# Kernel tuning notes

Measured on AMD Instinct MI355X. Metric: run time of the kernel, lower is better.

Reference implementation:

```python
import jax, jax.numpy as jnp
import numpy as np
import math

HEADS = 4
KV = 960
CH = (64, 128, 256, 512)
B, H, W = 8, 32, 32
EPS_IN = 1e-5  # nn.InstanceNorm2d default eps


def conv2d(x, w, groups=1, pad=0):
    # x: [N,C,H,W], w: [O, C//groups, kh, kw]
    return jax.lax.conv_general_dilated(
        x, w, (1, 1), [(pad, pad), (pad, pad)],
        feature_group_count=groups,
        dimension_numbers=('NCHW', 'OIHW', 'NCHW'))


def l2norm(x):
    # torch F.normalize(dim=-1): x / max(||x||_2, 1e-12)
    return x / jnp.maximum(jnp.linalg.norm(x, axis=-1, keepdims=True), 1e-12)


def setup_inputs() -> dict:
    key = jax.random.key(0)
    ks = iter(jax.random.split(key, 40))
    s = 0.02
    d = {}
    for i, c in enumerate(CH, 1):
        d[f'emb{i}'] = jax.random.normal(next(ks), (B, c, H, W), jnp.float32)
    d['emb_all'] = jax.random.normal(next(ks), (B, KV, H, W), jnp.float32)
    for i, c in enumerate(CH, 1):
        d[f'Wm{i}'] = jax.random.normal(next(ks), (c * HEADS, c, 1, 1), jnp.float32) * s
        # grouped 3x3: groups = c*HEADS//2 -> 2 in-channels per group
        d[f'Wq{i}'] = jax.random.normal(next(ks), (c * HEADS, 2, 3, 3), jnp.float32) * s
        d[f'Wp{i}'] = jax.random.normal(next(ks), (c, c, 1, 1), jnp.float32) * s
    d['Wmk'] = jax.random.normal(next(ks), (KV * HEADS, KV, 1, 1), jnp.float32) * s
    d['Wmv'] = jax.random.normal(next(ks), (KV * HEADS, KV, 1, 1), jnp.float32) * s
    # depthwise 3x3: groups = KV*HEADS
    d['Wk'] = jax.random.normal(next(ks), (KV * HEADS, 1, 3, 3), jnp.float32) * s
    d['Wv'] = jax.random.normal(next(ks), (KV * HEADS, 1, 3, 3), jnp.float32) * s
    return d


def _forward(emb1, emb2, emb3, emb4, emb_all,
             Wm1, Wq1, Wp1, Wm2, Wq2, Wp2, Wm3, Wq3, Wp3, Wm4, Wq4, Wp4,
             Wmk, Wmv, Wk, Wv):
    b, _, h, w = emb1.shape
    hw = h * w
    # shared K/V: 1x1 multi-head expand then depthwise 3x3
    k = conv2d(conv2d(emb_all, Wmk), Wk, groups=KV * HEADS, pad=1)
    v = conv2d(conv2d(emb_all, Wmv), Wv, groups=KV * HEADS, pad=1)
    k = l2norm(k.reshape(b, HEADS, KV, hw))   # [b,H,KV,hw]
    v = v.reshape(b, HEADS, KV, hw)
    scale = 1.0 / math.sqrt(KV)
    outs = []
    for emb, Wm, Wq, Wp in ((emb1, Wm1, Wq1, Wp1), (emb2, Wm2, Wq2, Wp2),
                            (emb3, Wm3, Wq3, Wp3), (emb4, Wm4, Wq4, Wp4)):
        c = emb.shape[1]
        q = conv2d(conv2d(emb, Wm), Wq, groups=c * HEADS // 2, pad=1)
        q = l2norm(q.reshape(b, HEADS, c, hw))            # [b,H,c,hw]
        attn = jnp.einsum('bhcn,bhdn->bhcd', q, k) * scale  # [b,H,c,KV]
        # InstanceNorm2d over (c, KV) per (b, head), no affine, biased var
        mu = attn.mean(axis=(2, 3), keepdims=True)
        var = attn.var(axis=(2, 3), keepdims=True)
        probs = jax.nn.softmax((attn - mu) / jnp.sqrt(var + EPS_IN), axis=-1)
        # dropout rate 0 (inference) -> identity
        out = jnp.einsum('bhcd,bhdn->bhcn', probs, v).mean(axis=1)  # head-mean -> [b,c,hw]
        outs.append(conv2d(out.reshape(b, c, h, w), Wp))
    return tuple(outs)


def reference(emb1, emb2, emb3, emb4, emb_all,
              Wm1, Wq1, Wp1, Wm2, Wq2, Wp2, Wm3, Wq3, Wp3, Wm4, Wq4, Wp4,
              Wmk, Wmv, Wk, Wv):
    return _forward(emb1, emb2, emb3, emb4, emb_all,
                    Wm1, Wq1, Wp1, Wm2, Wq2, Wp2, Wm3, Wq3, Wp3, Wm4, Wq4, Wp4,
                    Wmk, Wmv, Wk, Wv)
```

## Files before the change

kernel.cpp:

```cpp
#include <hip/hip_runtime.h>
#include <hip/hip_bf16.h>
#include <math.h>

typedef __hip_bfloat16 bf16;
typedef __attribute__((ext_vector_type(8))) short short8;
typedef __attribute__((ext_vector_type(8))) unsigned short u16x8;
typedef __attribute__((ext_vector_type(4))) float f32x4;
typedef long long ll;

#define B_ 8
#define HEADS_ 4
#define KV_ 960
#define HW_ 1024
#define CKV_ 3840

__device__ __forceinline__ float wredsum(float v) {
#pragma unroll
  for (int o = 32; o > 0; o >>= 1) v += __shfl_xor(v, o);
  return v;
}
__device__ __forceinline__ float wredmax(float v) {
#pragma unroll
  for (int o = 32; o > 0; o >>= 1) v = fmaxf(v, __shfl_xor(v, o));
  return v;
}

__device__ __forceinline__ float bfu2f(unsigned short u) {
  union { unsigned int i; float f; } c;
  c.i = ((unsigned int)u) << 16;
  return c.f;
}
__device__ __forceinline__ unsigned short f2bfu(float f) {
  bf16 h = __float2bfloat16(f);
  return *(unsigned short*)&h;
}

__device__ __forceinline__ void gl_lds16(const void* g, void* l) {
  __builtin_amdgcn_global_load_lds(
      (const __attribute__((address_space(1))) unsigned*)g,
      (__attribute__((address_space(3))) unsigned*)l, 16, 0, 0);
}

__global__ void __launch_bounds__(256) castw(const float* __restrict__ in,
                                             bf16* __restrict__ out, int n) {
  int i = (blockIdx.x * 256 + threadIdx.x) * 4;
  if (i < n) {
    float4 v = *(const float4*)(in + i);
    out[i] = __float2bfloat16(v.x);
    out[i + 1] = __float2bfloat16(v.y);
    out[i + 2] = __float2bfloat16(v.z);
    out[i + 3] = __float2bfloat16(v.w);
  }
}

template <typename InT>
__global__ void __launch_bounds__(256) tcast(const InT* __restrict__ in,
                                             bf16* __restrict__ out, int R,
                                             ll inZ, ll outZ) {
  __shared__ float t[32][33];
  const int x = threadIdx.x & 31, y0 = threadIdx.x >> 5;
  const int c0 = blockIdx.x << 5, r0 = blockIdx.y << 5;
  const InT* ip = in + (ll)blockIdx.z * inZ + (ll)r0 * 1024 + c0;
  bf16* op = out + (ll)blockIdx.z * outZ + (ll)c0 * R + r0;
#pragma unroll
  for (int i = 0; i < 4; i++) {
    int r = y0 + i * 8;
    float v;
    if constexpr (__is_same(InT, float)) v = ip[(ll)r * 1024 + x];
    else v = __bfloat162float(ip[(ll)r * 1024 + x]);
    t[r][x] = v;
  }
  __syncthreads();
#pragma unroll
  for (int i = 0; i < 4; i++) {
    int cc = y0 + i * 8;
    op[(ll)cc * R + x] = __float2bfloat16(t[x][cc]);
  }
}

template <int OUTMODE, bool STATS>
__global__ void __launch_bounds__(256) gemm_mfma(
    const bf16* __restrict__ A, const bf16* __restrict__ Bt, void* __restrict__ Y,
    int M, int N, int K, int nh,
    ll aZ, ll aH, ll bZ, ll bH, ll yZ, int ldy, float scale,
    float* __restrict__ part) {
  __shared__ bf16 As[2][128 * 32];
  __shared__ bf16 Bs[2][128 * 32];
  __shared__ float rs1[4], rs2[4];
  const int tid = threadIdx.x;
  const int lane = tid & 63;
  const int wave = tid >> 6;
  const int wr = wave >> 1, wc = wave & 1;

  const int gy = gridDim.y, gz = gridDim.z;
  int orig = (blockIdx.z * gy + blockIdx.y) * 8 + blockIdx.x;
  int cpx = (gy * gz);
  int flat = (orig & 7) * cpx + (orig >> 3);
  const int lx = flat & 7;
  int rest = flat >> 3;
  const int ly = rest % gy;
  const int lz = rest / gy;

  const int z = lz;
  const int m0 = ly << 7, n0 = lx << 7;

  f32x4 acc[4][4];
#pragma unroll
  for (int i = 0; i < 4; i++)
#pragma unroll
    for (int j = 0; j < 4; j++) acc[i][j] = (f32x4){0.f, 0.f, 0.f, 0.f};

  const int frow = lane & 15;
  const int kq = lane >> 4;

  const bf16* Ah = A + (ll)z * aZ;
  const bf16* Bh = Bt + (ll)z * bZ;
  int k0n = 0;

  auto stage = [&](int buf) {
#pragma unroll
    for (int t = 0; t < 2; t++) {
      const int e = (wave * 2 + t) * 64 + lane;
      const int row = e >> 2;
      const int ks = (e & 3) ^ ((row >> 1) & 3);
      int gr = m0 + row; gr = gr < M ? gr : M - 1;
      gl_lds16(Ah + (ll)gr * K + k0n + ks * 8,
               (char*)&As[buf][0] + (wave * 2 + t) * 1024);
      int rn = n0 + row; rn = rn < N ? rn : N - 1;
      gl_lds16(Bh + (ll)rn * K + k0n + ks * 8,
               (char*)&Bs[buf][0] + (wave * 2 + t) * 1024);
    }
  };

  const int kpt = K >> 5;
  const int iters = nh * kpt;
  stage(0);
  __syncthreads();

  int buf = 0;
  for (int it = 0; it < iters; ++it) {
    if (it + 1 < iters) {
      k0n += 32;
      if (k0n == K) { k0n = 0; Ah += aH; Bh += bH; }
      stage(buf ^ 1);
    }
    short8 af[4], bfr[4];
#pragma unroll
    for (int fm = 0; fm < 4; fm++) {
      const int row = wr * 64 + fm * 16 + frow;
      af[fm] = *(const short8*)&As[buf][((row << 2) | (kq ^ ((row >> 1) & 3))) << 3];
    }
#pragma unroll
    for (int fn = 0; fn < 4; fn++) {
      const int row = wc * 64 + fn * 16 + frow;
      bfr[fn] = *(const short8*)&Bs[buf][((row << 2) | (kq ^ ((row >> 1) & 3))) << 3];
    }
#pragma unroll
    for (int fm = 0; fm < 4; fm++)
#pragma unroll
      for (int fn = 0; fn < 4; fn++)
        acc[fm][fn] = __builtin_amdgcn_mfma_f32_16x16x32_bf16(
            af[fm], bfr[fn], acc[fm][fn], 0, 0, 0);
    __syncthreads();
    buf ^= 1;
  }

  const int rq = kq << 2;
  float lsum = 0.f, lsq = 0.f;
#pragma unroll
  for (int fm = 0; fm < 4; fm++) {
    const int mrow = m0 + wr * 64 + fm * 16 + rq;
#pragma unroll
    for (int fn = 0; fn < 4; fn++) {
      const int ncol = n0 + wc * 64 + fn * 16 + frow;
      if (ncol >= N) continue;
      if constexpr (OUTMODE == 0) {
        float* Yp = (float*)Y + (ll)z * yZ;
#pragma unroll
        for (int i = 0; i < 4; i++)
          if (mrow + i < M) {
            float v = acc[fm][fn][i] * scale;
            Yp[(ll)(mrow + i) * ldy + ncol] = v;
            if constexpr (STATS) { lsum += v; lsq += v * v; }
          }
      } else if constexpr (OUTMODE == 1) {
        bf16* Yp = (bf16*)Y + (ll)z * yZ;
#pragma unroll
        for (int i = 0; i < 4; i++)
          if (mrow + i < M)
            Yp[(ll)(mrow + i) * ldy + ncol] =
                __float2bfloat16(acc[fm][fn][i] * scale);
      } else {
        if (mrow < M) {
          bf16* Yp = (bf16*)Y + (ll)z * yZ + (ll)ncol * ldy + mrow;
#pragma unroll
          for (int i = 0; i < 4; i++)
            Yp[i] = __float2bfloat16(acc[fm][fn][i] * scale);
        }
      }
    }
  }
  if constexpr (STATS) {
    lsum = wredsum(lsum);
    lsq = wredsum(lsq);
    if (lane == 0) { rs1[wave] = lsum; rs2[wave] = lsq; }
    __syncthreads();
    if (tid == 0) {
      int slot = ly * 8 + lx;
      part[((ll)z * 32 + slot) * 2] = rs1[0] + rs1[1] + rs1[2] + rs1[3];
      part[((ll)z * 32 + slot) * 2 + 1] = rs2[0] + rs2[1] + rs2[2] + rs2[3];
    }
  }
}

template <int OUTMODE, bool STATS>
__global__ void __launch_bounds__(512, 2) gemm8(
    const bf16* __restrict__ A, const bf16* __restrict__ Bt, void* __restrict__ Y,
    int M, int N, int K, int nh,
    ll aZ, ll aH, ll bZ, ll bH, ll yZ, int ldy, float scale,
    float* __restrict__ part) {
  __shared__ char lds[131072];
  __shared__ float rs1[8], rs2[8];
  const int tid = threadIdx.x;
  const int lane = tid & 63;
  const int wave = tid >> 6;
  const int wm = wave >> 2, wn = wave & 3;

  const int nx = gridDim.x, my = gridDim.y;
  const int nwg = nx * my * gridDim.z;
  int orig = (blockIdx.z * my + blockIdx.y) * nx + blockIdx.x;
  int q8 = nwg >> 3, r8 = nwg & 7;
  int xcd = orig & 7, bidx = orig >> 3;
  int flat = (xcd < r8) ? xcd * (q8 + 1) + bidx
                        : r8 * (q8 + 1) + (xcd - r8) * q8 + bidx;
  const int lx = flat % nx;
  int rest = flat / nx;
  const int ly = rest % my;
  const int lz = rest / my;

  const int m0 = ly << 8, n0 = lx << 8;
  const int ktiles = K >> 6;
  const int nt = nh * ktiles;

  f32x4 acc[8][4];
#pragma unroll
  for (int i = 0; i < 8; i++)
#pragma unroll
    for (int j = 0; j < 4; j++) acc[i][j] = (f32x4){0.f, 0.f, 0.f, 0.f};

  const int frow = lane & 15;
  const int kq = lane >> 4;
  const int swz = frow & 7;

  auto stageRound = [&](int matB, int r, int tt, int buf) {
    int h = tt / ktiles;
    int koff = (tt % ktiles) << 6;
    int s = (r << 9) + tid;
    int row = s >> 3;
    int ks = (s & 7) ^ (row & 7);
    const bf16* src;
    char* dst;
    if (!matB) {
      int gr = m0 + row; gr = gr < M ? gr : M - 1;
      src = A + (ll)lz * aZ + (ll)h * aH + (ll)gr * K + koff + (ks << 3);
      dst = lds + buf * 32768 + (((r << 3) + wave) << 10);
    } else {
      int gr = n0 + row; gr = gr < N ? gr : N - 1;
      src = Bt + (ll)lz * bZ + (ll)h * bH + (ll)gr * K + koff + (ks << 3);
      dst = lds + 65536 + buf * 32768 + (((r << 3) + wave) << 10);
    }
    gl_lds16(src, dst);
  };

  auto readA = [&](int fm, int kh, int cur) -> short8 {
    int row = wm * 128 + fm * 16 + frow;
    int slot = (kq + (kh << 2)) ^ swz;
    return *(const short8*)(lds + cur * 32768 + row * 128 + slot * 16);
  };
  auto readB = [&](int fn, int kh, int cur) -> short8 {
    int row = wn * 64 + fn * 16 + frow;
    int slot = (kq + (kh << 2)) ^ swz;
    return *(const short8*)(lds + 65536 + cur * 32768 + row * 128 + slot * 16);
  };

  stageRound(1, 0, 0, 0); stageRound(1, 1, 0, 0);
  stageRound(1, 2, 0, 0); stageRound(1, 3, 0, 0);
  stageRound(0, 0, 0, 0); stageRound(0, 2, 0, 0);
  stageRound(0, 1, 0, 0); stageRound(0, 3, 0, 0);

  int cur = 0;
  for (int tt = 0; tt < nt; ++tt) {
    const bool hasNext = (tt + 1 < nt);
    short8 bfr[4][2];
#pragma unroll
    for (int p = 0; p < 4; p++) {
      if (p == 0) {
        if (hasNext) asm volatile("s_waitcnt vmcnt(2)" ::: "memory");
        else         asm volatile("s_waitcnt vmcnt(0)" ::: "memory");
        __builtin_amdgcn_s_barrier();
        __builtin_amdgcn_sched_barrier(0);
#pragma unroll
        for (int fn = 0; fn < 4; fn++)
#pragma unroll
          for (int kh = 0; kh < 2; kh++) bfr[fn][kh] = readB(fn, kh, cur);
      }
      if (p == 2) {
        if (hasNext) asm volatile("s_waitcnt vmcnt(4)" ::: "memory");
        __builtin_amdgcn_s_barrier();
        __builtin_amdgcn_sched_barrier(0);
      }
      short8 a0k0 = readA(2 * p, 0, cur), a0k1 = readA(2 * p, 1, cur);
      short8 a1k0 = readA(2 * p + 1, 0, cur), a1k1 = readA(2 * p + 1, 1, cur);
      if (hasNext) {
        if (p == 0) { stageRound(1, 0, tt + 1, cur ^ 1); stageRound(1, 1, tt + 1, cur ^ 1); }
        else if (p == 1) { stageRound(1, 2, tt + 1, cur ^ 1); stageRound(1, 3, tt + 1, cur ^ 1); }
        else if (p == 2) { stageRound(0, 0, tt + 1, cur ^ 1); stageRound(0, 2, tt + 1, cur ^ 1); }
        else { stageRound(0, 1, tt + 1, cur ^ 1); stageRound(0, 3, tt + 1, cur ^ 1); }
      }
      __builtin_amdgcn_s_setprio(1);
#pragma unroll
      for (int fn = 0; fn < 4; fn++) {
        acc[2 * p][fn] = __builtin_amdgcn_mfma_f32_16x16x32_bf16(
            a0k0, bfr[fn][0], acc[2 * p][fn], 0, 0, 0);
        acc[2 * p][fn] = __builtin_amdgcn_mfma_f32_16x16x32_bf16(
            a0k1, bfr[fn][1], acc[2 * p][fn], 0, 0, 0);
        acc[2 * p + 1][fn] = __builtin_amdgcn_mfma_f32_16x16x32_bf16(
            a1k0, bfr[fn][0], acc[2 * p + 1][fn], 0, 0, 0);
        acc[2 * p + 1][fn] = __builtin_amdgcn_mfma_f32_16x16x32_bf16(
            a1k1, bfr[fn][1], acc[2 * p + 1][fn], 0, 0, 0);
      }
      __builtin_amdgcn_s_setprio(0);
    }
    cur ^= 1;
  }

  const int rq = kq << 2;
  float lsum = 0.f, lsq = 0.f;
#pragma unroll
  for (int fm = 0; fm < 8; fm++) {
    const int mrow = m0 + wm * 128 + fm * 16 + rq;
#pragma unroll
    for (int fn = 0; fn < 4; fn++) {
      const int ncol = n0 + wn * 64 + fn * 16 + frow;
      if (ncol >= N) continue;
      if constexpr (OUTMODE == 0) {
        float* Yp = (float*)Y + (ll)lz * yZ;
#pragma unroll
        for (int i = 0; i < 4; i++)
          if (mrow + i < M) {
            float v = acc[fm][fn][i] * scale;
            Yp[(ll)(mrow + i) * ldy + ncol] = v;
            if constexpr (STATS) { lsum += v; lsq += v * v; }
          }
      } else if constexpr (OUTMODE == 1) {
        bf16* Yp = (bf16*)Y + (ll)lz * yZ;
#pragma unroll
        for (int i = 0; i < 4; i++)
          if (mrow + i < M)
            Yp[(ll)(mrow + i) * ldy + ncol] =
                __float2bfloat16(acc[fm][fn][i] * scale);
      } else {
        if (mrow < M) {
          bf16* Yp = (bf16*)Y + (ll)lz * yZ + (ll)ncol * ldy + mrow;
#pragma unroll
          for (int i = 0; i < 4; i++)
            Yp[i] = __float2bfloat16(acc[fm][fn][i] * scale);
        }
      }
    }
  }
  if constexpr (STATS) {
    lsum = wredsum(lsum);
    lsq = wredsum(lsq);
    if (lane == 0) { rs1[wave] = lsum; rs2[wave] = lsq; }
    __syncthreads();
    if (tid == 0) {
      float s = 0.f, s2 = 0.f;
#pragma unroll
      for (int w = 0; w < 8; w++) { s += rs1[w]; s2 += rs2[w]; }
      int slot = ly * nx + lx;
      part[((ll)lz * 32 + slot) * 2] = s;
      part[((ll)lz * 32 + slot) * 2 + 1] = s2;
    }
  }
}

__global__ void __launch_bounds__(256) pv_reduce(const bf16* __restrict__ part,
                                                 bf16* __restrict__ out,
                                                 int planeShift) {
  const ll idx = ((ll)blockIdx.x * 256 + threadIdx.x) * 4;
  const int b = (int)(idx >> planeShift);
  const ll off = idx - ((ll)b << planeShift);
  const bf16* base = part + (((ll)b * 4) << planeShift) + off;
  float a0 = 0.f, a1 = 0.f, a2 = 0.f, a3 = 0.f;
#pragma unroll
  for (int s = 0; s < 4; s++) {
    ushort4 u = *(const ushort4*)(base + ((ll)s << planeShift));
    a0 += bfu2f(u.x); a1 += bfu2f(u.y); a2 += bfu2f(u.z); a3 += bfu2f(u.w);
  }
  ushort4 o;
  o.x = f2bfu(a0 * 0.25f);
  o.y = f2bfu(a1 * 0.25f);
  o.z = f2bfu(a2 * 0.25f);
  o.w = f2bfu(a3 * 0.25f);
  *(ushort4*)(out + idx) = o;
}

template <bool NORM>
__global__ void __launch_bounds__(256) dw3x3v(const bf16* __restrict__ in,
                                              const float* __restrict__ w9,
                                              bf16* __restrict__ out, int C) {
  __shared__ float tile[34][36];
  __shared__ float red[4];
  const int bc = blockIdx.x;
  const int ch = bc % C;
  const int tid = threadIdx.x;
  const int y = tid >> 3;
  const int x0 = (tid & 7) << 2;
  const bf16* ip = in + ((size_t)bc << 10);

  ushort4 u = *(const ushort4*)(ip + (y << 5) + x0);
  tile[y + 1][x0 + 1] = bfu2f(u.x);
  tile[y + 1][x0 + 2] = bfu2f(u.y);
  tile[y + 1][x0 + 3] = bfu2f(u.z);
  tile[y + 1][x0 + 4] = bfu2f(u.w);
  if (tid < 34) { tile[0][tid] = 0.f; tile[33][tid] = 0.f; }
  if (tid < 32) { tile[tid + 1][0] = 0.f; tile[tid + 1][33] = 0.f; }
  __syncthreads();

  const float* wc = w9 + ch * 9;
  float s[4] = {0.f, 0.f, 0.f, 0.f};
#pragma unroll
  for (int dy = 0; dy < 3; dy++) {
    const float* tr = &tile[y + dy][x0];
    float c0 = tr[0], c1 = tr[1], c2 = tr[2], c3 = tr[3], c4 = tr[4], c5 = tr[5];
    float wa = wc[dy * 3], wb = wc[dy * 3 + 1], wd = wc[dy * 3 + 2];
    s[0] += c0 * wa + c1 * wb + c2 * wd;
    s[1] += c1 * wa + c2 * wb + c3 * wd;
    s[2] += c2 * wa + c3 * wb + c4 * wd;
    s[3] += c3 * wa + c4 * wb + c5 * wd;
  }

  float inv = 1.f;
  if (NORM) {
    float ss = s[0] * s[0] + s[1] * s[1] + s[2] * s[2] + s[3] * s[3];
    ss = wredsum(ss);
    const int lane = tid & 63, wid = tid >> 6;
    if (lane == 0) red[wid] = ss;
    __syncthreads();
    inv = 1.0f / fmaxf(sqrtf(red[0] + red[1] + red[2] + red[3]), 1e-12f);
  }
  ushort4 o4;
  o4.x = f2bfu(s[0] * inv);
  o4.y = f2bfu(s[1] * inv);
  o4.z = f2bfu(s[2] * inv);
  o4.w = f2bfu(s[3] * inv);
  *(ushort4*)(out + ((size_t)bc << 10) + (y << 5) + x0) = o4;
}

__global__ void __launch_bounds__(256) dwtcast(const bf16* __restrict__ in,
                                               const float* __restrict__ w9,
                                               bf16* __restrict__ out) {
  __shared__ float t[3][32][34];
  const int jt = blockIdx.x;
  const int y = blockIdx.y;
  const int bh = blockIdx.z;
  const int b = bh >> 2, h = bh & 3;
  const int j0 = jt << 5;
  const int tid = threadIdx.x;

  if (tid < 192) {
    const int rr = tid / 64;
    const int rem = tid - rr * 64;
    const int jc = rem >> 1;
    const int half = rem & 1;
    const int iy = y - 1 + rr;
    float* dstp = &t[rr][jc][1 + (half << 4)];
    if (iy < 0 || iy > 31) {
#pragma unroll
      for (int u = 0; u < 16; u++) dstp[u] = 0.f;
    } else {
      const bf16* src = in + (((ll)b * CKV_ + h * KV_ + j0 + jc) << 10) +
                        (iy << 5) + (half << 4);
      u16x8 v0 = *(const u16x8*)src;
      u16x8 v1 = *(const u16x8*)(src + 8);
#pragma unroll
      for (int u = 0; u < 8; u++) dstp[u] = bfu2f(v0[u]);
#pragma unroll
      for (int u = 0; u < 8; u++) dstp[8 + u] = bfu2f(v1[u]);
    }
  }
  if (tid < 96) {
    const int rr = tid / 32, jc = tid - rr * 32;
    t[rr][jc][0] = 0.f;
    t[rr][jc][33] = 0.f;
  }
  __syncthreads();

  const int jp = tid & 15;
  const int xq = tid >> 4;
  const int ch0 = jp << 1;
  const float* wA = w9 + ((size_t)h * KV_ + j0 + ch0) * 9;
  const float* wB = wA + 9;

  bf16* orow = out + (ll)bh * 983040 + (ll)j0 + (ch0);
#pragma unroll
  for (int sx = 0; sx < 2; sx++) {
    const int x = xq + (sx << 4);
    float sA = 0.f, sB = 0.f;
#pragma unroll
    for (int dy = 0; dy < 3; dy++) {
      const float* rA = &t[dy][ch0][x];
      const float* rB = &t[dy][ch0 + 1][x];
      sA += rA[0] * wA[dy * 3] + rA[1] * wA[dy * 3 + 1] + rA[2] * wA[dy * 3 + 2];
      sB += rB[0] * wB[dy * 3] + rB[1] * wB[dy * 3 + 1] + rB[2] * wB[dy * 3 + 2];
    }
    const int n = (y << 5) + x;
    ushort2 o;
    o.x = f2bfu(sA);
    o.y = f2bfu(sB);
    *(ushort2*)(orow + (ll)n * 960) = o;
  }
}

__global__ void __launch_bounds__(256) gq3x3v(const bf16* __restrict__ in,
                                              const float* __restrict__ wq,
                                              bf16* __restrict__ out, int C4) {
  __shared__ float t0[34][36];
  __shared__ float t1[34][36];
  __shared__ float red[4];
  const int bo = blockIdx.x;
  const int o = bo % C4;
  const int b = bo / C4;
  const int ic0 = (o >> 1) << 1;
  const int tid = threadIdx.x;
  const int y = tid >> 3;
  const int x0 = (tid & 7) << 2;
  const bf16* p0 = in + (((size_t)b * C4 + ic0) << 10);

  ushort4 u0 = *(const ushort4*)(p0 + (y << 5) + x0);
  ushort4 u1 = *(const ushort4*)(p0 + 1024 + (y << 5) + x0);
  t0[y + 1][x0 + 1] = bfu2f(u0.x);
  t0[y + 1][x0 + 2] = bfu2f(u0.y);
  t0[y + 1][x0 + 3] = bfu2f(u0.z);
  t0[y + 1][x0 + 4] = bfu2f(u0.w);
  t1[y + 1][x0 + 1] = bfu2f(u1.x);
  t1[y + 1][x0 + 2] = bfu2f(u1.y);
  t1[y + 1][x0 + 3] = bfu2f(u1.z);
  t1[y + 1][x0 + 4] = bfu2f(u1.w);
  if (tid < 34) {
    t0[0][tid] = 0.f; t0[33][tid] = 0.f;
    t1[0][tid] = 0.f; t1[33][tid] = 0.f;
  }
  if (tid < 32) {
    t0[tid + 1][0] = 0.f; t0[tid + 1][33] = 0.f;
    t1[tid + 1][0] = 0.f; t1[tid + 1][33] = 0.f;
  }
  __syncthreads();

  const float* w = wq + o * 18;
  float s[4] = {0.f, 0.f, 0.f, 0.f};
#pragma unroll
  for (int dy = 0; dy < 3; dy++) {
    {
      const float* tr = &t0[y + dy][x0];
      float c0 = tr[0], c1 = tr[1], c2 = tr[2], c3 = tr[3], c4 = tr[4], c5 = tr[5];
      float wa = w[dy * 3], wb = w[dy * 3 + 1], wd = w[dy * 3 + 2];
      s[0] += c0 * wa + c1 * wb + c2 * wd;
      s[1] += c1 * wa + c2 * wb + c3 * wd;
      s[2] += c2 * wa + c3 * wb + c4 * wd;
      s[3] += c3 * wa + c4 * wb + c5 * wd;
    }
    {
      const float* tr = &t1[y + dy][x0];
      float c0 = tr[0], c1 = tr[1], c2 = tr[2], c3 = tr[3], c4 = tr[4], c5 = tr[5];
      float wa = w[9 + dy * 3], wb = w[9 + dy * 3 + 1], wd = w[9 + dy * 3 + 2];
      s[0] += c0 * wa + c1 * wb + c2 * wd;
      s[1] += c1 * wa + c2 * wb + c3 * wd;
      s[2] += c2 * wa + c3 * wb + c4 * wd;
      s[3] += c3 * wa + c4 * wb + c5 * wd;
    }
  }

  float ss = s[0] * s[0] + s[1] * s[1] + s[2] * s[2] + s[3] * s[3];
  ss = wredsum(ss);
  const int lane = tid & 63, wid = tid >> 6;
  if (lane == 0) red[wid] = ss;
  __syncthreads();
  float inv = 1.0f / fmaxf(sqrtf(red[0] + red[1] + red[2] + red[3]), 1e-12f);

  ushort4 o4;
  o4.x = f2bfu(s[0] * inv);
  o4.y = f2bfu(s[1] * inv);
  o4.z = f2bfu(s[2] * inv);
  o4.w = f2bfu(s[3] * inv);
  *(ushort4*)(out + ((size_t)bo << 10) + (y << 5) + x0) = o4;
}

__global__ void __launch_bounds__(256) softmax_rows(const float* __restrict__ attn,
                                                    const float* __restrict__ part,
                                                    int nslots,
                                                    bf16* __restrict__ probs, int c) {
  __shared__ float rm[4], rs[4];
  const int row = blockIdx.x;
  const int bh = row / c;
  const float* p = attn + (size_t)row * 960;
  bf16* op = probs + (size_t)row * 960;
  const int tid = threadIdx.x;

  float s = 0.f, s2 = 0.f;
  for (int i = 0; i < nslots; i++) {
    s += part[((ll)bh * 32 + i) * 2];
    s2 += part[((ll)bh * 32 + i) * 2 + 1];
  }
  const float n = (float)(c * 960);
  const float mu = s / n;
  const float var = s2 / n - mu * mu;
  const float rstd = rsqrtf(var + 1e-5f);

  float v[4];
  float mx = -1e30f;
#pragma unroll
  for (int u = 0; u < 4; u++) {
    int j = tid + (u << 8);
    if (j < 960) {
      v[u] = (p[j] - mu) * rstd;
      mx = fmaxf(mx, v[u]);
    } else {
      v[u] = -1e30f;
    }
  }
  mx = wredmax(mx);
  const int lane = tid & 63, wid = tid >> 6;
  if (lane == 0) rm[wid] = mx;
  __syncthreads();
  mx = fmaxf(fmaxf(rm[0], rm[1]), fmaxf(rm[2], rm[3]));

  float sum = 0.f;
#pragma unroll
  for (int u = 0; u < 4; u++) {
    int j = tid + (u << 8);
    if (j < 960) {
      v[u] = __expf(v[u] - mx);
      sum += v[u];
    }
  }
  sum = wredsum(sum);
  if (lane == 0) rs[wid] = sum;
  __syncthreads();
  sum = rs[0] + rs[1] + rs[2] + rs[3];
  const float inv = 1.0f / sum;
#pragma unroll
  for (int u = 0; u < 4; u++) {
    int j = tid + (u << 8);
    if (j < 960) op[j] = __float2bfloat16(v[u] * inv);
  }
}

static size_t p4_size(int nb) {
  const int chunkB = (nb + 1) / 2;
  size_t a = (size_t)nb * 4194304;
  size_t b = (size_t)nb * 1966080 + 7372800;
  size_t c = (size_t)chunkB * 7864320;
  size_t m = a > b ? a : b;
  return m > c ? m : c;
}
static size_t p5_size(int nb) {
  size_t a = (size_t)nb * 1048576;
  return a > 7372800 ? a : 7372800;
}
static size_t total_need(int nb) {
  return 3 * (size_t)nb * 7864320 + p4_size(nb) + p5_size(nb) + 3490816;
}

static void run_group(const float* const emb[4], const float* emb_all,
                      const float* const Wq[4],
                      const float* Wmk, const float* Wmv,
                      const float* Wk, const float* Wv,
                      bf16* Wm_all, bf16* Wp_all,
                      float* out, const size_t* out_off,
                      char* ws, int nb, hipStream_t stream) {
  const size_t szBig = (size_t)nb * 7864320;
  char* P1 = ws;
  char* P2 = P1 + szBig;
  char* P3 = P2 + szBig;
  char* P4 = P3 + szBig;
  char* P5 = P4 + p4_size(nb);
  char* FX = P5 + p5_size(nb);

  bf16* kbuf = (bf16*)P1;
  bf16* vt   = (bf16*)P2;
  bf16* kvexp = (bf16*)P3;
  float* attnb = (float*)P3;
  bf16* pvpart = (bf16*)P3;
  bf16* embT_all = (bf16*)P4;
  bf16* Wmv_bf = (bf16*)(P4 + (size_t)nb * 1966080);
  bf16* qbuf = (bf16*)P4;
  bf16* probsb = (bf16*)P4;
  bf16* Wmk_bf = (bf16*)P5;
  bf16* OtT = (bf16*)P5;
  float* part = (float*)(FX + 3482112);

  const float qk_scale = 1.0f / sqrtf((float)KV_);
  const int CHs[4] = {64, 128, 256, 512};
  const size_t wm_off[4] = {0, 16384, 81920, 344064};
  const size_t wp_off[4] = {0, 4096, 20480, 86016};

  castw<<<3600, 256, 0, stream>>>(Wmk, Wmk_bf, 3686400);
  castw<<<3600, 256, 0, stream>>>(Wmv, Wmv_bf, 3686400);
  tcast<float><<<dim3(32, 30, nb), 256, 0, stream>>>(emb_all, embT_all, 960,
                                                     983040LL, 983040LL);
  gemm8<1, false><<<dim3(4, 15, nb), 512, 0, stream>>>(
      Wmk_bf, embT_all, kvexp, 3840, 1024, 960, 1, 0, 0, 983040LL, 0,
      3932160LL, 1024, 1.f, nullptr);
  dw3x3v<true><<<nb * CKV_, 256, 0, stream>>>(kvexp, Wk, kbuf, CKV_);
  gemm8<1, false><<<dim3(4, 15, nb), 512, 0, stream>>>(
      Wmv_bf, embT_all, kvexp, 3840, 1024, 960, 1, 0, 0, 983040LL, 0,
      3932160LL, 1024, 1.f, nullptr);
  dwtcast<<<dim3(30, 32, nb * 4), 256, 0, stream>>>(kvexp, Wv, vt);

  for (int br = 0; br < 4; br++) {
    const int c = CHs[br];
    const int C4 = c * 4;
    const int mtiles = (c + 127) / 128;
    bf16* Wm_bf = Wm_all + wm_off[br];
    bf16* Wp_bf = Wp_all + wp_off[br];
    int planeShift = 10;
    for (int t = c; t > 1; t >>= 1) planeShift++;

    tcast<float><<<dim3(32, c / 32, nb), 256, 0, stream>>>(
        emb[br], qbuf, c, (ll)c * 1024, (ll)c * 1024);
    if (c == 512) {
      gemm8<1, false><<<dim3(4, C4 / 256, nb), 512, 0, stream>>>(
          Wm_bf, qbuf, kvexp, C4, 1024, c, 1, 0, 0, (ll)c * 1024, 0,
          (ll)C4 * 1024, 1024, 1.f, nullptr);
    } else {
      gemm_mfma<1, false><<<dim3(8, C4 / 128, nb), 256, 0, stream>>>(
          Wm_bf, qbuf, kvexp, C4, 1024, c, 1, 0, 0, (ll)c * 1024, 0,
          (ll)C4 * 1024, 1024, 1.f, nullptr);
    }
    gq3x3v<<<nb * C4, 256, 0, stream>>>(kvexp, Wq[br], qbuf, C4);
    int nslots;
    if (c == 512) {
      gemm8<0, true><<<dim3(4, c / 256, nb * 4), 512, 0, stream>>>(
          qbuf, kbuf, attnb, c, 960, 1024, 1, (ll)c * 1024, 0, 983040LL, 0,
          (ll)c * 960, 960, qk_scale, part);
      nslots = (c / 256) * 4;
    } else {
      gemm_mfma<0, true><<<dim3(8, mtiles, nb * 4), 256, 0, stream>>>(
          qbuf, kbuf, attnb, c, 960, 1024, 1, (ll)c * 1024, 0, 983040LL, 0,
          (ll)c * 960, 960, qk_scale, part);
      nslots = mtiles * 8;
    }
    softmax_rows<<<nb * 4 * c, 256, 0, stream>>>(attnb, part, nslots, probsb, c);
    if (c == 512) {
      gemm8<2, false><<<dim3(4, c / 256, nb * 4), 512, 0, stream>>>(
          probsb, vt, pvpart, c, 1024, 960, 1, (ll)c * 960, 0, 983040LL, 0,
          (ll)1024 * c, c, 1.f, nullptr);
    } else {
      gemm_mfma<2, false><<<dim3(8, mtiles, nb * 4), 256, 0, stream>>>(
          probsb, vt, pvpart, c, 1024, 960, 1, (ll)c * 960, 0, 983040LL, 0,
          (ll)1024 * c, c, 1.f, nullptr);
    }
    pv_reduce<<<nb * c, 256, 0, stream>>>(pvpart, OtT, planeShift);
    gemm_mfma<0, false><<<dim3(8, mtiles, nb), 256, 0, stream>>>(
        Wp_bf, OtT, out + out_off[br], c, 1024, c, 1, 0, 0,
        (ll)1024 * c, 0, (ll)c * 1024, 1024, 1.f, nullptr);
  }
}

extern "C" void kernel_launch(void* const* d_in, const int* in_sizes, int n_in,
                              void* d_out, int out_size, void* d_ws, size_t ws_size,
                              hipStream_t stream) {
  const float* emb[4] = {(const float*)d_in[0], (const float*)d_in[1],
                         (const float*)d_in[2], (const float*)d_in[3]};
  const float* emb_all = (const float*)d_in[4];
  const float* Wm[4] = {(const float*)d_in[5], (const float*)d_in[8],
                        (const float*)d_in[11], (const float*)d_in[14]};
  const float* Wq[4] = {(const float*)d_in[6], (const float*)d_in[9],
                        (const float*)d_in[12], (const float*)d_in[15]};
  const float* Wp[4] = {(const float*)d_in[7], (const float*)d_in[10],
                        (const float*)d_in[13], (const float*)d_in[16]};
  const float* Wmk = (const float*)d_in[17];
  const float* Wmv = (const float*)d_in[18];
  const float* Wk = (const float*)d_in[19];
  const float* Wv = (const float*)d_in[20];
  float* out = (float*)d_out;

  const int CHs[4] = {64, 128, 256, 512};
  const size_t out_off_full[4] = {0, 524288, 1572864, 3670016};
  const size_t wm_off[4] = {0, 16384, 81920, 344064};
  const size_t wp_off[4] = {0, 4096, 20480, 86016};

  int nb = 1;
  if (ws_size >= total_need(8)) nb = 8;
  else if (ws_size >= total_need(4)) nb = 4;
  else if (ws_size >= total_need(2)) nb = 2;

  char* FX = (char*)d_ws + 3 * (size_t)nb * 7864320 + p4_size(nb) + p5_size(nb);
  bf16* Wm_all = (bf16*)FX;
  bf16* Wp_all = (bf16*)(FX + 2785280);

  for (int br = 0; br < 4; br++) {
    const int c = CHs[br];
    castw<<<(4 * c * c / 4 + 255) / 256, 256, 0, stream>>>(
        Wm[br], Wm_all + wm_off[br], 4 * c * c);
    castw<<<(c * c / 4 + 255) / 256, 256, 0, stream>>>(
        Wp[br], Wp_all + wp_off[br], c * c);
  }

  for (int b0 = 0; b0 < B_; b0 += nb) {
    const float* embB[4];
    for (int i = 0; i < 4; i++) embB[i] = emb[i] + (size_t)b0 * CHs[i] * HW_;
    const float* emb_allB = emb_all + (size_t)b0 * KV_ * HW_;
    size_t out_offB[4];
    for (int i = 0; i < 4; i++)
      out_offB[i] = out_off_full[i] + (size_t)b0 * CHs[i] * HW_;
    run_group(embB, emb_allB, Wq, Wmk, Wmv, Wk, Wv, Wm_all, Wp_all,
              out, out_offB, (char*)d_ws, nb, stream);
  }
}
```

Before: 810.0 us.

## Restructure GEMM LDS tiles into K-half quarters with new swizzle and pipeline

The 256x256x64 bf16 GEMM main loop now splits each K tile into two 32-wide halves, each stored in its own LDS region with 64-byte rows and a different XOR swizzle. Each half is staged with two async global-to-LDS loads per matrix, and the loop waits and barriers once per half, then issues 32 MFMAs per half. The aim is a more regular load/compute interleave and conflict-free LDS reads with fewer barrier phases. In exchange it holds 12 fragments in registers at once and changes the vmcnt accounting, which could add register pressure or stalls.

```diff
diff --git a/kernel.cpp b/kernel.cpp
--- a/kernel.cpp
+++ b/kernel.cpp
@@ -250,88 +250,66 @@
 
   const int frow = lane & 15;
   const int kq = lane >> 4;
-  const int swz = frow & 7;
-
-  auto stageRound = [&](int matB, int r, int tt, int buf) {
+  const int rswz = (frow >> 1) & 3;
+
+  auto stageQ = [&](int matB, int kh, int tt, int buf) {
     int h = tt / ktiles;
-    int koff = (tt % ktiles) << 6;
-    int s = (r << 9) + tid;
-    int row = s >> 3;
-    int ks = (s & 7) ^ (row & 7);
-    const bf16* src;
-    char* dst;
-    if (!matB) {
-      int gr = m0 + row; gr = gr < M ? gr : M - 1;
-      src = A + (ll)lz * aZ + (ll)h * aH + (ll)gr * K + koff + (ks << 3);
-      dst = lds + buf * 32768 + (((r << 3) + wave) << 10);
-    } else {
-      int gr = n0 + row; gr = gr < N ? gr : N - 1;
-      src = Bt + (ll)lz * bZ + (ll)h * bH + (ll)gr * K + koff + (ks << 3);
-      dst = lds + 65536 + buf * 32768 + (((r << 3) + wave) << 10);
-    }
-    gl_lds16(src, dst);
+    int koff = ((tt % ktiles) << 6) + (kh << 5);
+#pragma unroll
+    for (int r = 0; r < 2; r++) {
+      int s = (r << 9) + tid;
+      int row = s >> 2;
+      int kc = (s & 3) ^ ((row >> 1) & 3);
+      if (!matB) {
+        int gr = m0 + row; gr = gr < M ? gr : M - 1;
+        gl_lds16(A + (ll)lz * aZ + (ll)h * aH + (ll)gr * K + koff + (kc << 3),
+                 lds + buf * 32768 + (kh << 14) + (r << 13) + (tid << 4));
+      } else {
+        int gr = n0 + row; gr = gr < N ? gr : N - 1;
+        gl_lds16(Bt + (ll)lz * bZ + (ll)h * bH + (ll)gr * K + koff + (kc << 3),
+                 lds + 65536 + buf * 32768 + (kh << 14) + (r << 13) + (tid << 4));
+      }
+    }
   };
 
-  auto readA = [&](int fm, int kh, int cur) -> short8 {
+  auto readA = [&](int fm, int kh, int buf) -> short8 {
     int row = wm * 128 + fm * 16 + frow;
-    int slot = (kq + (kh << 2)) ^ swz;
-    return *(const short8*)(lds + cur * 32768 + row * 128 + slot * 16);
+    int kc = kq ^ rswz;
+    return *(const short8*)(lds + buf * 32768 + (kh << 14) + row * 64 + (kc << 4));
   };
-  auto readB = [&](int fn, int kh, int cur) -> short8 {
+  auto readB = [&](int fn, int kh, int buf) -> short8 {
     int row = wn * 64 + fn * 16 + frow;
-    int slot = (kq + (kh << 2)) ^ swz;
-    return *(const short8*)(lds + 65536 + cur * 32768 + row * 128 + slot * 16);
+    int kc = kq ^ rswz;
+    return *(const short8*)(lds + 65536 + buf * 32768 + (kh << 14) + row * 64 + (kc << 4));
   };
 
-  stageRound(1, 0, 0, 0); stageRound(1, 1, 0, 0);
-  stageRound(1, 2, 0, 0); stageRound(1, 3, 0, 0);
-  stageRound(0, 0, 0, 0); stageRound(0, 2, 0, 0);
-  stageRound(0, 1, 0, 0); stageRound(0, 3, 0, 0);
-
-  int cur = 0;
+  stageQ(0, 0, 0, 0); stageQ(1, 0, 0, 0);
+  stageQ(0, 1, 0, 0); stageQ(1, 1, 0, 0);
+
   for (int tt = 0; tt < nt; ++tt) {
+    const int buf = tt & 1;
     const bool hasNext = (tt + 1 < nt);
-    short8 bfr[4][2];
-#pragma unroll
-    for (int p = 0; p < 4; p++) {
-      if (p == 0) {
-        if (hasNext) asm volatile("s_waitcnt vmcnt(2)" ::: "memory");
-        else         asm volatile("s_waitcnt vmcnt(0)" ::: "memory");
-        __builtin_amdgcn_s_barrier();
-        __builtin_amdgcn_sched_barrier(0);
+#pragma unroll
+    for (int kh = 0; kh < 2; kh++) {
+      if (hasNext || kh == 0) asm volatile("s_waitcnt vmcnt(4)" ::: "memory");
+      else                    asm volatile("s_waitcnt vmcnt(0)" ::: "memory");
+      __builtin_amdgcn_s_barrier();
+      __builtin_amdgcn_sched_barrier(0);
+      short8 af[8], bf4[4];
+#pragma unroll
+      for (int fm = 0; fm < 8; fm++) af[fm] = readA(fm, kh, buf);
+#pragma unroll
+      for (int fn = 0; fn < 4; fn++) bf4[fn] = readB(fn, kh, buf);
+      if (hasNext) { stageQ(0, kh, tt + 1, buf ^ 1); stageQ(1, kh, tt + 1, buf ^ 1); }
+      __builtin_amdgcn_s_setprio(1);
+#pragma unroll
+      for (int fm = 0; fm < 8; fm++)
 #pragma unroll
         for (int fn = 0; fn < 4; fn++)
-#pragma unroll
-          for (int kh = 0; kh < 2; kh++) bfr[fn][kh] = readB(fn, kh, cur);
-      }
-      if (p == 2) {
-        if (hasNext) asm volatile("s_waitcnt vmcnt(4)" ::: "memory");
-        __builtin_amdgcn_s_barrier();
-        __builtin_amdgcn_sched_barrier(0);
-      }
-      short8 a0k0 = readA(2 * p, 0, cur), a0k1 = readA(2 * p, 1, cur);
-      short8 a1k0 = readA(2 * p + 1, 0, cur), a1k1 = readA(2 * p + 1, 1, cur);
-      if (hasNext) {
-        if (p == 0) { stageRound(1, 0, tt + 1, cur ^ 1); stageRound(1, 1, tt + 1, cur ^ 1); }
-        else if (p == 1) { stageRound(1, 2, tt + 1, cur ^ 1); stageRound(1, 3, tt + 1, cur ^ 1); }
-        else if (p == 2) { stageRound(0, 0, tt + 1, cur ^ 1); stageRound(0, 2, tt + 1, cur ^ 1); }
-        else { stageRound(0, 1, tt + 1, cur ^ 1); stageRound(0, 3, tt + 1, cur ^ 1); }
-      }
-      __builtin_amdgcn_s_setprio(1);
-#pragma unroll
-      for (int fn = 0; fn < 4; fn++) {
-        acc[2 * p][fn] = __builtin_amdgcn_mfma_f32_16x16x32_bf16(
-            a0k0, bfr[fn][0], acc[2 * p][fn], 0, 0, 0);
-        acc[2 * p][fn] = __builtin_amdgcn_mfma_f32_16x16x32_bf16(
-            a0k1, bfr[fn][1], acc[2 * p][fn], 0, 0, 0);
-        acc[2 * p + 1][fn] = __builtin_amdgcn_mfma_f32_16x16x32_bf16(
-            a1k0, bfr[fn][0], acc[2 * p + 1][fn], 0, 0, 0);
-        acc[2 * p + 1][fn] = __builtin_amdgcn_mfma_f32_16x16x32_bf16(
-            a1k1, bfr[fn][1], acc[2 * p + 1][fn], 0, 0, 0);
-      }
+          acc[fm][fn] = __builtin_amdgcn_mfma_f32_16x16x32_bf16(
+              af[fm], bf4[fn], acc[fm][fn], 0, 0, 0);
       __builtin_amdgcn_s_setprio(0);
     }
-    cur ^= 1;
   }
 
   const int rq = kq << 2;
```

After: 819.0 us. No clear change (+1.1%).
